# Kernel optimization log

Hardware: AMD Instinct MI355X
Metric: run time of the kernel (lower is better)

## Reference

```python
import jax, jax.numpy as jnp
import numpy as np

T, B, N, C = 4, 4, 4096, 512
H = 8
D = C // H            # head_dim = 64
TAU = 2.0             # LIF tau
VTH = 1.0             # LIF threshold


def lif_spike(x):
    # LIFNode called once from zero state: v = 0 + (x - 0)/tau; spike = v >= vth
    v = x / TAU
    return (v >= VTH).astype(x.dtype)


def setup_inputs() -> dict:
    key = jax.random.key(0)
    ks = jax.random.split(key, 9)
    s = 0.05  # weight scale so pre-spike potentials straddle the threshold
    x = jax.random.normal(ks[0], (T, B, N, C), dtype=jnp.float32)
    Wq = jax.random.normal(ks[1], (C, C), dtype=jnp.float32) * s
    bq = jnp.zeros((C,), dtype=jnp.float32)
    Wk = jax.random.normal(ks[2], (C, C), dtype=jnp.float32) * s
    bk = jnp.zeros((C,), dtype=jnp.float32)
    Wv = jax.random.normal(ks[3], (C, C), dtype=jnp.float32) * s
    bv = jnp.zeros((C,), dtype=jnp.float32)
    Wo = jax.random.normal(ks[4], (C, C), dtype=jnp.float32) * s
    bo = jnp.zeros((C,), dtype=jnp.float32)
    return {"x": x, "Wq": Wq, "bq": bq, "Wk": Wk, "bk": bk,
            "Wv": Wv, "bv": bv, "Wo": Wo, "bo": bo}


def reference(x, Wq, bq, Wk, bk, Wv, bv, Wo, bo):
    # nn.Linear: y = x @ W.T + b (SeqToANNContainer just flattens (T,B))
    q = jnp.einsum('tbnc,oc->tbno', x, Wq) + bq
    k = jnp.einsum('tbnc,oc->tbno', x, Wk) + bk
    v = jnp.einsum('tbnc,oc->tbno', x, Wv) + bv
    # reshape to heads; attention runs over the spiking time axis T per token
    q = q.reshape(T, B, N, H, D).transpose(1, 2, 0, 3, 4)   # (B,N,T,H,D)
    k = k.reshape(T, B, N, H, D).transpose(1, 2, 3, 4, 0)   # (B,N,H,D,T)
    v = v.reshape(T, B, N, H, D).transpose(1, 2, 3, 0, 4)   # (B,N,H,T,D)
    attn = jnp.einsum('bnthd,bnhds->bnths', q, k) / jnp.sqrt(jnp.float32(D))
    attn = lif_spike(attn)                                  # binary spikes replace softmax
    out = jnp.einsum('bnths,bnhsd->bnthd', attn, v)         # (B,N,T,H,D)
    out = out.transpose(2, 0, 1, 3, 4).reshape(T, B, N, C)
    return jnp.einsum('tbnc,oc->tbno', out, Wo) + bo
```

## Files before the change

kernel.cpp:

```cpp
#include <hip/hip_runtime.h>

#define PTOT  16384
#define CCC   512
#define HHH   8
#define NK1   32
#define NK2   16

typedef __attribute__((ext_vector_type(4)))  float f32x4;
typedef __attribute__((ext_vector_type(16))) float f32x16;
typedef _Float16 half_t;
typedef __attribute__((ext_vector_type(8))) _Float16 f16x8;

#define MFMA16(a,b,c) __builtin_amdgcn_mfma_f32_16x16x32_f16(a,b,c,0,0,0)
#define MFMA32(a,b,c) __builtin_amdgcn_mfma_f32_32x32x16_f16(a,b,c,0,0,0)

#define XH_OFF   ((size_t)0)
#define XL_OFF   ((size_t)33554432)
#define ACT_OFF  ((size_t)67108864)
#define W_OFF    ((size_t)100663296)
#define WPL      ((size_t)262144)

__device__ __forceinline__ size_t blk_off16(int row, int col) {
    return ((size_t)((row >> 4) * 16 + (col >> 5)) << 9)
         + (size_t)(((((col >> 3) & 3) * 16) + (row & 15)) << 3) + (col & 7);
}

__global__ void k0_split(const float* __restrict__ x,
                         const float* __restrict__ Wq, const float* __restrict__ Wk,
                         const float* __restrict__ Wv, const float* __restrict__ Wo,
                         half_t* __restrict__ ws)
{
    const int u = blockIdx.x * 256 + threadIdx.x;
    if (u < 4194304) {
        const int f = u >> 6, lane6 = u & 63;
        const int grow32 = f >> 5, ktc = f & 31;
        const int row = grow32 * 32 + (lane6 & 31);
        const int k   = ktc * 16 + (lane6 >> 5) * 8;
        const float4 a = *(const float4*)(x + (size_t)row * CCC + k);
        const float4 b = *(const float4*)(x + (size_t)row * CCC + k + 4);
        const float e[8] = {a.x, a.y, a.z, a.w, b.x, b.y, b.z, b.w};
        f16x8 vh8, vl8;
        #pragma unroll
        for (int d = 0; d < 8; ++d) {
            const half_t hi = (half_t)e[d];
            vh8[d] = hi; vl8[d] = (half_t)(e[d] - (float)hi);
        }
        const size_t off = ((size_t)f << 9) + lane6 * 8;
        *(f16x8*)(ws + XH_OFF + off) = vh8;
        *(f16x8*)(ws + XL_OFF + off) = vl8;
        return;
    }
    const int u2  = u - 4194304;
    const int mat = u2 >> 15, r = u2 & 32767;
    if (mat < 3) {
        const float* src = (mat == 0) ? Wq : (mat == 1) ? Wk : Wv;
        const int f = r >> 6, lane6 = r & 63;
        const int grow32 = f >> 5, ktc = f & 31;
        const int row = grow32 * 32 + (lane6 & 31);
        const int k   = ktc * 16 + (lane6 >> 5) * 8;
        const float4 a = *(const float4*)(src + (size_t)row * CCC + k);
        const float4 b = *(const float4*)(src + (size_t)row * CCC + k + 4);
        const float e[8] = {a.x, a.y, a.z, a.w, b.x, b.y, b.z, b.w};
        f16x8 vh8, vl8;
        #pragma unroll
        for (int d = 0; d < 8; ++d) {
            const half_t hi = (half_t)e[d];
            vh8[d] = hi; vl8[d] = (half_t)(e[d] - (float)hi);
        }
        const size_t off = ((size_t)f << 9) + lane6 * 8;
        half_t* dh = ws + W_OFF + (size_t)(mat * 2) * WPL;
        *(f16x8*)(dh + off) = vh8;
        if (mat < 2) *(f16x8*)(dh + WPL + off) = vl8;
        return;
    }
    const int gr = r >> 10, v = r & 1023;
    const int ktc = v >> 6, chunk = (v >> 4) & 3, i = v & 15;
    const int row = gr * 16 + i, col = ktc * 32 + chunk * 8;
    const float4 a = *(const float4*)(Wo + (size_t)row * CCC + col);
    const float4 b = *(const float4*)(Wo + (size_t)row * CCC + col + 4);
    const float e[8] = {a.x, a.y, a.z, a.w, b.x, b.y, b.z, b.w};
    f16x8 vh8;
    #pragma unroll
    for (int d = 0; d < 8; ++d) vh8[d] = (half_t)e[d];
    *(f16x8*)(ws + W_OFF + 5 * WPL + blk_off16(row, col)) = vh8;
}

__global__ __launch_bounds__(256, 3)
void k1_mfma(const half_t* __restrict__ ws,
             const float* __restrict__ bq, const float* __restrict__ bk,
             const float* __restrict__ bv,
             half_t* __restrict__ acth)
{
    __shared__ __align__(16) char smem[52224];

    const int tid  = threadIdx.x;
    const int lane = tid & 63;
    const int wv   = tid >> 6;
    const int rg   = wv >> 1;
    const int cg   = wv & 1;
    const int l31  = lane & 31;
    const int l5   = lane >> 5;

    const int xcd  = blockIdx.x & 7;
    const int rest = blockIdx.x >> 3;
    const int h    = rest & 7;
    const int tg   = rest >> 3;
    const int p0   = (tg * 8 + xcd) * 32;

    const int cnt  = (wv < 2) ? 5 : 4;
    const int base = (wv < 2) ? wv * 5 : 2 + wv * 4;
    const half_t* gb[5]; int lo_[5];
    #pragma unroll
    for (int ii = 0; ii < 5; ++ii) {
        const int i = base + ii;
        size_t eoff; int loff;
        if (i < 8) {
            const int t = i >> 1, pl = i & 1;
            const size_t rbg = (size_t)t * 512 + (p0 >> 5);
            eoff = (pl ? XL_OFF : XH_OFF) + (rbg << 14) + lane * 8;
            loff = i * 1024;
        } else {
            const int s = (i - 8) & 15;
            const int plw = (s >> 1) > 4 ? 4 : (s >> 1), cb = s & 1;
            eoff = W_OFF + (size_t)plw * WPL + ((size_t)(h * 2 + cb) << 14) + lane * 8;
            loff = 8192 + s * 1024;
        }
        gb[ii] = ws + eoff;
        lo_[ii] = loff;
    }

#define K1_STAGE(buf, kt) do {                                                  \
    _Pragma("unroll")                                                           \
    for (int ii = 0; ii < 5; ++ii)                                              \
        if (ii < cnt)                                                           \
            __builtin_amdgcn_global_load_lds(                                   \
                (const __attribute__((address_space(1))) void*)(gb[ii] + (size_t)(kt) * 512), \
                (__attribute__((address_space(3))) void*)(smem + (buf) * 18432 + lo_[ii]),    \
                16, 0, 0);                                                      \
    } while (0)

    f32x16 accQ[2], accK[2], accV[2];
    {
        const int c0 = h * 64 + cg * 32 + l31;
        const float q0 = bq[c0], k0 = bk[c0], v0 = bv[c0];
        #pragma unroll
        for (int i = 0; i < 16; ++i) {
            accQ[0][i] = q0; accQ[1][i] = q0;
            accK[0][i] = k0; accK[1][i] = k0;
            accV[0][i] = v0; accV[1][i] = v0;
        }
    }

    K1_STAGE(0, 0);

    #pragma unroll 2
    for (int kt = 0; kt < NK1; ++kt) {
        const int cur = kt & 1;
        if (kt + 1 < NK1) {
            K1_STAGE(cur ^ 1, kt + 1);
            if (cnt == 5) asm volatile("s_waitcnt vmcnt(5)" ::: "memory");
            else          asm volatile("s_waitcnt vmcnt(4)" ::: "memory");
        } else {
            asm volatile("s_waitcnt vmcnt(0)" ::: "memory");
        }
        __builtin_amdgcn_sched_barrier(0);
        __builtin_amdgcn_s_barrier();

        const char* bp = smem + cur * 18432;
        const int boff = 8192 + cg * 1024 + lane * 16;
        const int t0 = rg * 2, t1 = rg * 2 + 1;

        const f16x8 Ah0 = *(const f16x8*)(bp + (t0 * 2 + 0) * 1024 + lane * 16);
        const f16x8 Al0 = *(const f16x8*)(bp + (t0 * 2 + 1) * 1024 + lane * 16);
        const f16x8 Ah1 = *(const f16x8*)(bp + (t1 * 2 + 0) * 1024 + lane * 16);
        const f16x8 Al1 = *(const f16x8*)(bp + (t1 * 2 + 1) * 1024 + lane * 16);
        const f16x8 Bqh = *(const f16x8*)(bp + boff);
        const f16x8 Bql = *(const f16x8*)(bp + boff + 2048);
        asm volatile("s_waitcnt lgkmcnt(0)" ::: "memory");
        __builtin_amdgcn_sched_barrier(0);
        __builtin_amdgcn_s_setprio(1);
        accQ[0] = MFMA32(Ah0, Bqh, accQ[0]);
        accQ[1] = MFMA32(Ah1, Bqh, accQ[1]);
        accQ[0] = MFMA32(Ah0, Bql, accQ[0]);
        accQ[1] = MFMA32(Ah1, Bql, accQ[1]);
        accQ[0] = MFMA32(Al0, Bqh, accQ[0]);
        accQ[1] = MFMA32(Al1, Bqh, accQ[1]);
        __builtin_amdgcn_s_setprio(0);
        __builtin_amdgcn_s_barrier();

        const f16x8 Bkh = *(const f16x8*)(bp + boff + 4096);
        const f16x8 Bkl = *(const f16x8*)(bp + boff + 6144);
        const f16x8 Bvh = *(const f16x8*)(bp + boff + 8192);
        asm volatile("s_waitcnt lgkmcnt(0)" ::: "memory");
        __builtin_amdgcn_sched_barrier(0);
        __builtin_amdgcn_s_setprio(1);
        accK[0] = MFMA32(Ah0, Bkh, accK[0]);
        accK[1] = MFMA32(Ah1, Bkh, accK[1]);
        accV[0] = MFMA32(Ah0, Bvh, accV[0]);
        accV[1] = MFMA32(Ah1, Bvh, accV[1]);
        accK[0] = MFMA32(Ah0, Bkl, accK[0]);
        accK[1] = MFMA32(Ah1, Bkl, accK[1]);
        accK[0] = MFMA32(Al0, Bkh, accK[0]);
        accK[1] = MFMA32(Al1, Bkh, accK[1]);
        __builtin_amdgcn_s_setprio(0);
        __builtin_amdgcn_s_barrier();
        __builtin_amdgcn_sched_barrier(0);
    }

    float* qa = (float*)smem;
    float* ka = qa + 4352;
    float* va = qa + 8704;

    const int ar  = tid >> 2;
    const int t_  = ar >> 4;
    const int jj  = ar & 15;
    const int sub = tid & 3;

    #pragma unroll
    for (int hh = 0; hh < 2; ++hh) {
        #pragma unroll
        for (int rf = 0; rf < 2; ++rf) {
            const int t = rg * 2 + rf;
            #pragma unroll
            for (int rr = 0; rr < 8; ++rr) {
                const int reg = hh * 8 + rr;
                const int j2  = (rr & 3) + 8 * (rr >> 2) + 4 * l5;
                const int idx = (t * 16 + j2) * 68 + cg * 32 + l31;
                qa[idx] = accQ[rf][reg];
                ka[idx] = accK[rf][reg];
                va[idx] = accV[rf][reg];
            }
        }
        __syncthreads();

        const float* qp = qa + ar * 68 + sub * 16;
        const float4 q0 = *(const float4*)(qp);
        const float4 q1 = *(const float4*)(qp + 4);
        const float4 q2 = *(const float4*)(qp + 8);
        const float4 q3 = *(const float4*)(qp + 12);
        float sc[4];
        #pragma unroll
        for (int ss = 0; ss < 4; ++ss) {
            const float* kp = ka + (ss * 16 + jj) * 68 + sub * 16;
            const float4 k0 = *(const float4*)(kp);
            const float4 k1 = *(const float4*)(kp + 4);
            const float4 k2 = *(const float4*)(kp + 8);
            const float4 k3 = *(const float4*)(kp + 12);
            float p = q0.x*k0.x + q0.y*k0.y + q0.z*k0.z + q0.w*k0.w
                    + q1.x*k1.x + q1.y*k1.y + q1.z*k1.z + q1.w*k1.w
                    + q2.x*k2.x + q2.y*k2.y + q2.z*k2.z + q2.w*k2.w
                    + q3.x*k3.x + q3.y*k3.y + q3.z*k3.z + q3.w*k3.w;
            p += __shfl_xor(p, 1);
            p += __shfl_xor(p, 2);
            sc[ss] = p;
        }
        float o[16];
        #pragma unroll
        for (int d = 0; d < 16; ++d) o[d] = 0.f;
        #pragma unroll
        for (int ss = 0; ss < 4; ++ss) {
            if (sc[ss] >= 16.0f) {
                const float* vp = va + (ss * 16 + jj) * 68 + sub * 16;
                const float4 v0 = *(const float4*)(vp);
                const float4 v1 = *(const float4*)(vp + 4);
                const float4 v2 = *(const float4*)(vp + 8);
                const float4 v3 = *(const float4*)(vp + 12);
                o[0]+=v0.x; o[1]+=v0.y; o[2]+=v0.z;  o[3]+=v0.w;
                o[4]+=v1.x; o[5]+=v1.y; o[6]+=v1.z;  o[7]+=v1.w;
                o[8]+=v2.x; o[9]+=v2.y; o[10]+=v2.z; o[11]+=v2.w;
                o[12]+=v3.x;o[13]+=v3.y;o[14]+=v3.z; o[15]+=v3.w;
            }
        }
        f16x8 o0, o1;
        #pragma unroll
        for (int d = 0; d < 8; ++d) { o0[d] = (half_t)o[d]; o1[d] = (half_t)o[d + 8]; }
        const int grow = t_ * 1024 + (p0 >> 4) + hh;
        const int colb = h * 64 + sub * 16;
        const size_t cbase = ((size_t)(grow * 16 + (colb >> 5))) << 9;
        const int c0 = (colb >> 3) & 3;
        *(f16x8*)(acth + cbase + (size_t)((c0       * 16 + jj) << 3)) = o0;
        *(f16x8*)(acth + cbase + (size_t)(((c0 + 1) * 16 + jj) << 3)) = o1;
        __syncthreads();
    }
#undef K1_STAGE
}

__global__ __launch_bounds__(256, 4)
void k2_gemm(const half_t* __restrict__ acth, const half_t* __restrict__ oh,
             const float* __restrict__ bo, float* __restrict__ out)
{
    __shared__ __align__(16) char smem[32768];

    const int tid  = threadIdx.x;
    const int lane = tid & 63;
    const int wv   = tid >> 6;
    const int wr   = wv >> 1, wc = wv & 1;
    const int l15  = lane & 15, l4 = lane >> 4;
    const int bn   = (blockIdx.x & 3) * 128;
    const int bm   = (blockIdx.x >> 2) * 128;

    const half_t* gb[4]; int lo_[4];
    #pragma unroll
    for (int ii = 0; ii < 4; ++ii) {
        const int i = wv * 4 + ii;
        if (i < 8) {
            const int grow = (bm >> 4) + i;
            gb[ii] = acth + ((size_t)grow << 13) + lane * 8;
            lo_[ii] = i * 1024;
        } else {
            const int fb = i - 8;
            const int grow = (bn >> 4) + fb;
            gb[ii] = oh + ((size_t)grow << 13) + lane * 8;
            lo_[ii] = 8192 + fb * 1024;
        }
    }

#define K2_STAGE(buf, kt) do {                                                  \
    _Pragma("unroll")                                                           \
    for (int ii = 0; ii < 4; ++ii)                                              \
        __builtin_amdgcn_global_load_lds(                                       \
            (const __attribute__((address_space(1))) void*)(gb[ii] + (size_t)(kt) * 512), \
            (__attribute__((address_space(3))) void*)(smem + (buf) * 16384 + lo_[ii]),    \
            16, 0, 0);                                                          \
    } while (0)

    f32x4 acc[4][4];
    #pragma unroll
    for (int rf = 0; rf < 4; ++rf)
        #pragma unroll
        for (int cf = 0; cf < 4; ++cf) acc[rf][cf] = f32x4{0.f, 0.f, 0.f, 0.f};

    K2_STAGE(0, 0);

    #pragma unroll
    for (int kt = 0; kt < NK2; ++kt) {
        const int cur = kt & 1;
        if (kt + 1 < NK2) {
            K2_STAGE(cur ^ 1, kt + 1);
            asm volatile("s_waitcnt vmcnt(4)" ::: "memory");
        } else {
            asm volatile("s_waitcnt vmcnt(0)" ::: "memory");
        }
        __builtin_amdgcn_sched_barrier(0);
        __builtin_amdgcn_s_barrier();

        const char* bp = smem + cur * 16384;
        f16x8 B[4];
        #pragma unroll
        for (int cf = 0; cf < 4; ++cf)
            B[cf] = *(const f16x8*)(bp + 8192 + (wc * 4 + cf) * 1024 + lane * 16);
        f16x8 A[4];
        #pragma unroll
        for (int rf = 0; rf < 4; ++rf)
            A[rf] = *(const f16x8*)(bp + (wr * 4 + rf) * 1024 + lane * 16);
        asm volatile("s_waitcnt lgkmcnt(0)" ::: "memory");
        __builtin_amdgcn_sched_barrier(0);
        __builtin_amdgcn_s_setprio(1);
        #pragma unroll
        for (int rf = 0; rf < 4; ++rf)
            #pragma unroll
            for (int cf = 0; cf < 4; ++cf)
                acc[rf][cf] = MFMA16(A[rf], B[cf], acc[rf][cf]);
        __builtin_amdgcn_s_setprio(0);
        __builtin_amdgcn_s_barrier();
        __builtin_amdgcn_sched_barrier(0);
    }

    float bo4[4];
    #pragma unroll
    for (int cf = 0; cf < 4; ++cf) bo4[cf] = bo[bn + (wc * 4 + cf) * 16 + l15];

    #pragma unroll
    for (int rf = 0; rf < 4; ++rf) {
        const int row0 = bm + (wr * 4 + rf) * 16 + l4 * 4;
        #pragma unroll
        for (int cf = 0; cf < 4; ++cf) {
            const int col = bn + (wc * 4 + cf) * 16 + l15;
            #pragma unroll
            for (int r = 0; r < 4; ++r)
                out[(size_t)(row0 + r) * CCC + col] = acc[rf][cf][r] + bo4[cf];
        }
    }
#undef K2_STAGE
}

extern "C" void kernel_launch(void* const* d_in, const int* in_sizes, int n_in,
                              void* d_out, int out_size, void* d_ws, size_t ws_size,
                              hipStream_t stream)
{
    const float* x  = (const float*)d_in[0];
    const float* Wq = (const float*)d_in[1];
    const float* bq = (const float*)d_in[2];
    const float* Wk = (const float*)d_in[3];
    const float* bk = (const float*)d_in[4];
    const float* Wv = (const float*)d_in[5];
    const float* bv = (const float*)d_in[6];
    const float* Wo = (const float*)d_in[7];
    const float* bo = (const float*)d_in[8];

    half_t* ws   = (half_t*)d_ws;
    half_t* acth = ws + ACT_OFF;
    float*  out  = (float*)d_out;

    hipLaunchKernelGGL(k0_split, dim3(16896), dim3(256), 0, stream,
                       x, Wq, Wk, Wv, Wo, ws);
    hipLaunchKernelGGL(k1_mfma, dim3(4096), dim3(256), 0, stream,
                       ws, bq, bk, bv, acth);
    hipLaunchKernelGGL(k2_gemm, dim3(2048), dim3(256), 0, stream,
                       acth, ws + W_OFF + 5*WPL, bo, out);
}
```

Baseline: 337.8 us.

## Software-pipeline LDS fragment reads with register double-buffering in both GEMM kernels

Restructures the main loops of the fused QKV kernel and the output projection GEMM. The next stage's LDS fragments are loaded into a second register set while MFMAs consume the current one, and the loop is unrolled by two with explicit waitcnt and barrier placement. This aims to hide LDS read latency behind matrix-core work. It doubles the fragment registers, so k2's launch bounds drop from 4 to 3 waves per SIMD, trading occupancy for pipelining.

```diff
diff --git a/kernel.cpp b/kernel.cpp
--- a/kernel.cpp
+++ b/kernel.cpp
@@ -139,6 +139,13 @@
                 16, 0, 0);                                                      \
     } while (0)
 
+#define VMW_CNT() do { if (cnt == 5) asm volatile("s_waitcnt vmcnt(5)" ::: "memory"); \
+                       else          asm volatile("s_waitcnt vmcnt(4)" ::: "memory"); } while (0)
+#define VMW_0()   asm volatile("s_waitcnt vmcnt(0)" ::: "memory")
+#define LGW_0()   asm volatile("s_waitcnt lgkmcnt(0)" ::: "memory")
+#define SCB()     __builtin_amdgcn_sched_barrier(0)
+#define SBAR()    __builtin_amdgcn_s_barrier()
+
     f32x16 accQ[2], accK[2], accV[2];
     {
         const int c0 = h * 64 + cg * 32 + l31;
@@ -151,62 +158,82 @@
         }
     }
 
+    const int boff = 8192 + cg * 1024 + lane * 16;
+    const int t0 = rg * 2, t1 = rg * 2 + 1;
+    const int aoff0 = (t0 * 2 + 0) * 1024 + lane * 16;
+    const int aoff1 = (t0 * 2 + 1) * 1024 + lane * 16;
+    const int aoff2 = (t1 * 2 + 0) * 1024 + lane * 16;
+    const int aoff3 = (t1 * 2 + 1) * 1024 + lane * 16;
+    const char* bp0 = smem;
+    const char* bp1 = smem + 18432;
+
+    f16x8 A0h0,A0l0,A0h1,A0l1,B0qh,B0ql,B0kh,B0kl,B0vh;
+    f16x8 A1h0,A1l0,A1h1,A1l1,B1qh,B1ql,B1kh,B1kl,B1vh;
+
+#define LOADSET0(bp) do { A0h0=*(const f16x8*)((bp)+aoff0); A0l0=*(const f16x8*)((bp)+aoff1); \
+    A0h1=*(const f16x8*)((bp)+aoff2); A0l1=*(const f16x8*)((bp)+aoff3);                       \
+    B0qh=*(const f16x8*)((bp)+boff); B0ql=*(const f16x8*)((bp)+boff+2048);                    \
+    B0kh=*(const f16x8*)((bp)+boff+4096); B0kl=*(const f16x8*)((bp)+boff+6144);               \
+    B0vh=*(const f16x8*)((bp)+boff+8192); } while (0)
+#define LOADSET1(bp) do { A1h0=*(const f16x8*)((bp)+aoff0); A1l0=*(const f16x8*)((bp)+aoff1); \
+    A1h1=*(const f16x8*)((bp)+aoff2); A1l1=*(const f16x8*)((bp)+aoff3);                       \
+    B1qh=*(const f16x8*)((bp)+boff); B1ql=*(const f16x8*)((bp)+boff+2048);                    \
+    B1kh=*(const f16x8*)((bp)+boff+4096); B1kl=*(const f16x8*)((bp)+boff+6144);               \
+    B1vh=*(const f16x8*)((bp)+boff+8192); } while (0)
+#define MM0() do {                                   \
+    accQ[0]=MFMA32(A0h0,B0qh,accQ[0]); accQ[1]=MFMA32(A0h1,B0qh,accQ[1]);  \
+    accK[0]=MFMA32(A0h0,B0kh,accK[0]); accK[1]=MFMA32(A0h1,B0kh,accK[1]);  \
+    accV[0]=MFMA32(A0h0,B0vh,accV[0]); accV[1]=MFMA32(A0h1,B0vh,accV[1]);  \
+    accQ[0]=MFMA32(A0h0,B0ql,accQ[0]); accQ[1]=MFMA32(A0h1,B0ql,accQ[1]);  \
+    accK[0]=MFMA32(A0h0,B0kl,accK[0]); accK[1]=MFMA32(A0h1,B0kl,accK[1]);  \
+    accQ[0]=MFMA32(A0l0,B0qh,accQ[0]); accQ[1]=MFMA32(A0l1,B0qh,accQ[1]);  \
+    accK[0]=MFMA32(A0l0,B0kh,accK[0]); accK[1]=MFMA32(A0l1,B0kh,accK[1]);  \
+    } while (0)
+#define MM1() do {                                   \
+    accQ[0]=MFMA32(A1h0,B1qh,accQ[0]); accQ[1]=MFMA32(A1h1,B1qh,accQ[1]);  \
+    accK[0]=MFMA32(A1h0,B1kh,accK[0]); accK[1]=MFMA32(A1h1,B1kh,accK[1]);  \
+    accV[0]=MFMA32(A1h0,B1vh,accV[0]); accV[1]=MFMA32(A1h1,B1vh,accV[1]);  \
+    accQ[0]=MFMA32(A1h0,B1ql,accQ[0]); accQ[1]=MFMA32(A1h1,B1ql,accQ[1]);  \
+    accK[0]=MFMA32(A1h0,B1kl,accK[0]); accK[1]=MFMA32(A1h1,B1kl,accK[1]);  \
+    accQ[0]=MFMA32(A1l0,B1qh,accQ[0]); accQ[1]=MFMA32(A1l1,B1qh,accQ[1]);  \
+    accK[0]=MFMA32(A1l0,B1kh,accK[0]); accK[1]=MFMA32(A1l1,B1kh,accK[1]);  \
+    } while (0)
+
     K1_STAGE(0, 0);
-
-    #pragma unroll 2
-    for (int kt = 0; kt < NK1; ++kt) {
-        const int cur = kt & 1;
-        if (kt + 1 < NK1) {
-            K1_STAGE(cur ^ 1, kt + 1);
-            if (cnt == 5) asm volatile("s_waitcnt vmcnt(5)" ::: "memory");
-            else          asm volatile("s_waitcnt vmcnt(4)" ::: "memory");
-        } else {
-            asm volatile("s_waitcnt vmcnt(0)" ::: "memory");
-        }
-        __builtin_amdgcn_sched_barrier(0);
-        __builtin_amdgcn_s_barrier();
-
-        const char* bp = smem + cur * 18432;
-        const int boff = 8192 + cg * 1024 + lane * 16;
-        const int t0 = rg * 2, t1 = rg * 2 + 1;
-
-        const f16x8 Ah0 = *(const f16x8*)(bp + (t0 * 2 + 0) * 1024 + lane * 16);
-        const f16x8 Al0 = *(const f16x8*)(bp + (t0 * 2 + 1) * 1024 + lane * 16);
-        const f16x8 Ah1 = *(const f16x8*)(bp + (t1 * 2 + 0) * 1024 + lane * 16);
-        const f16x8 Al1 = *(const f16x8*)(bp + (t1 * 2 + 1) * 1024 + lane * 16);
-        const f16x8 Bqh = *(const f16x8*)(bp + boff);
-        const f16x8 Bql = *(const f16x8*)(bp + boff + 2048);
-        asm volatile("s_waitcnt lgkmcnt(0)" ::: "memory");
-        __builtin_amdgcn_sched_barrier(0);
+    K1_STAGE(1, 1);
+    VMW_CNT();
+    SCB();
+    SBAR();
+    LOADSET0(bp0);
+
+    #pragma unroll 1
+    for (int kt = 0; kt < NK1; kt += 2) {
+        LGW_0(); SCB();
+        SBAR();
+        if (kt + 2 < NK1) K1_STAGE(0, kt + 2);
+        if (kt + 2 < NK1) { VMW_CNT(); } else { VMW_0(); }
+        SCB();
+        SBAR();
+        LOADSET1(bp1);
         __builtin_amdgcn_s_setprio(1);
-        accQ[0] = MFMA32(Ah0, Bqh, accQ[0]);
-        accQ[1] = MFMA32(Ah1, Bqh, accQ[1]);
-        accQ[0] = MFMA32(Ah0, Bql, accQ[0]);
-        accQ[1] = MFMA32(Ah1, Bql, accQ[1]);
-        accQ[0] = MFMA32(Al0, Bqh, accQ[0]);
-        accQ[1] = MFMA32(Al1, Bqh, accQ[1]);
+        MM0();
         __builtin_amdgcn_s_setprio(0);
-        __builtin_amdgcn_s_barrier();
-
-        const f16x8 Bkh = *(const f16x8*)(bp + boff + 4096);
-        const f16x8 Bkl = *(const f16x8*)(bp + boff + 6144);
-        const f16x8 Bvh = *(const f16x8*)(bp + boff + 8192);
-        asm volatile("s_waitcnt lgkmcnt(0)" ::: "memory");
-        __builtin_amdgcn_sched_barrier(0);
+
+        LGW_0(); SCB();
+        SBAR();
+        if (kt + 3 < NK1) K1_STAGE(1, kt + 3);
+        if (kt + 2 < NK1) {
+            if (kt + 3 < NK1) { VMW_CNT(); } else { VMW_0(); }
+            SCB();
+            SBAR();
+            LOADSET0(bp0);
+        }
         __builtin_amdgcn_s_setprio(1);
-        accK[0] = MFMA32(Ah0, Bkh, accK[0]);
-        accK[1] = MFMA32(Ah1, Bkh, accK[1]);
-        accV[0] = MFMA32(Ah0, Bvh, accV[0]);
-        accV[1] = MFMA32(Ah1, Bvh, accV[1]);
-        accK[0] = MFMA32(Ah0, Bkl, accK[0]);
-        accK[1] = MFMA32(Ah1, Bkl, accK[1]);
-        accK[0] = MFMA32(Al0, Bkh, accK[0]);
-        accK[1] = MFMA32(Al1, Bkh, accK[1]);
+        MM1();
         __builtin_amdgcn_s_setprio(0);
-        __builtin_amdgcn_s_barrier();
-        __builtin_amdgcn_sched_barrier(0);
-    }
-
+    }
+
+    __syncthreads();
     float* qa = (float*)smem;
     float* ka = qa + 4352;
     float* va = qa + 8704;
@@ -283,9 +310,13 @@
         __syncthreads();
     }
 #undef K1_STAGE
+#undef LOADSET0
+#undef LOADSET1
+#undef MM0
+#undef MM1
 }
 
-__global__ __launch_bounds__(256, 4)
+__global__ __launch_bounds__(256, 3)
 void k2_gemm(const half_t* __restrict__ acth, const half_t* __restrict__ oh,
              const float* __restrict__ bo, float* __restrict__ out)
 {
@@ -330,40 +361,73 @@
         #pragma unroll
         for (int cf = 0; cf < 4; ++cf) acc[rf][cf] = f32x4{0.f, 0.f, 0.f, 0.f};
 
+    const char* bp0 = smem;
+    const char* bp1 = smem + 16384;
+    f16x8 A0[4], B0[4], A1[4], B1[4];
+
+#define LOADS2_0(bp) do {                                                      \
+    _Pragma("unroll")                                                          \
+    for (int f = 0; f < 4; ++f) {                                              \
+        A0[f] = *(const f16x8*)((bp) + (wr * 4 + f) * 1024 + lane * 16);       \
+        B0[f] = *(const f16x8*)((bp) + 8192 + (wc * 4 + f) * 1024 + lane * 16);\
+    } } while (0)
+#define LOADS2_1(bp) do {                                                      \
+    _Pragma("unroll")                                                          \
+    for (int f = 0; f < 4; ++f) {                                              \
+        A1[f] = *(const f16x8*)((bp) + (wr * 4 + f) * 1024 + lane * 16);       \
+        B1[f] = *(const f16x8*)((bp) + 8192 + (wc * 4 + f) * 1024 + lane * 16);\
+    } } while (0)
+#define MM2_0() do {                                                           \
+    _Pragma("unroll")                                                          \
+    for (int rf = 0; rf < 4; ++rf)                                             \
+        _Pragma("unroll")                                                      \
+        for (int cf = 0; cf < 4; ++cf)                                         \
+            acc[rf][cf] = MFMA16(A0[rf], B0[cf], acc[rf][cf]);                 \
+    } while (0)
+#define MM2_1() do {                                                           \
+    _Pragma("unroll")                                                          \
+    for (int rf = 0; rf < 4; ++rf)                                             \
+        _Pragma("unroll")                                                      \
+        for (int cf = 0; cf < 4; ++cf)                                         \
+            acc[rf][cf] = MFMA16(A1[rf], B1[cf], acc[rf][cf]);                 \
+    } while (0)
+
     K2_STAGE(0, 0);
-
-    #pragma unroll
-    for (int kt = 0; kt < NK2; ++kt) {
-        const int cur = kt & 1;
-        if (kt + 1 < NK2) {
-            K2_STAGE(cur ^ 1, kt + 1);
-            asm volatile("s_waitcnt vmcnt(4)" ::: "memory");
-        } else {
-            asm volatile("s_waitcnt vmcnt(0)" ::: "memory");
-        }
+    K2_STAGE(1, 1);
+    asm volatile("s_waitcnt vmcnt(4)" ::: "memory");
+    __builtin_amdgcn_sched_barrier(0);
+    __builtin_amdgcn_s_barrier();
+    LOADS2_0(bp0);
+
+    #pragma unroll 1
+    for (int kt = 0; kt < NK2; kt += 2) {
+        asm volatile("s_waitcnt lgkmcnt(0)" ::: "memory");
         __builtin_amdgcn_sched_barrier(0);
         __builtin_amdgcn_s_barrier();
-
-        const char* bp = smem + cur * 16384;
-        f16x8 B[4];
-        #pragma unroll
-        for (int cf = 0; cf < 4; ++cf)
-            B[cf] = *(const f16x8*)(bp + 8192 + (wc * 4 + cf) * 1024 + lane * 16);
-        f16x8 A[4];
-        #pragma unroll
-        for (int rf = 0; rf < 4; ++rf)
-            A[rf] = *(const f16x8*)(bp + (wr * 4 + rf) * 1024 + lane * 16);
+        if (kt + 2 < NK2) K2_STAGE(0, kt + 2);
+        if (kt + 2 < NK2) asm volatile("s_waitcnt vmcnt(4)" ::: "memory");
+        else              asm volatile("s_waitcnt vmcnt(0)" ::: "memory");
+        __builtin_amdgcn_sched_barrier(0);
+        __builtin_amdgcn_s_barrier();
+        LOADS2_1(bp1);
+        __builtin_amdgcn_s_setprio(1);
+        MM2_0();
+        __builtin_amdgcn_s_setprio(0);
+
         asm volatile("s_waitcnt lgkmcnt(0)" ::: "memory");
         __builtin_amdgcn_sched_barrier(0);
+        __builtin_amdgcn_s_barrier();
+        if (kt + 3 < NK2) K2_STAGE(1, kt + 3);
+        if (kt + 2 < NK2) {
+            if (kt + 3 < NK2) asm volatile("s_waitcnt vmcnt(4)" ::: "memory");
+            else              asm volatile("s_waitcnt vmcnt(0)" ::: "memory");
+            __builtin_amdgcn_sched_barrier(0);
+            __builtin_amdgcn_s_barrier();
+            LOADS2_0(bp0);
+        }
         __builtin_amdgcn_s_setprio(1);
-        #pragma unroll
-        for (int rf = 0; rf < 4; ++rf)
-            #pragma unroll
-            for (int cf = 0; cf < 4; ++cf)
-                acc[rf][cf] = MFMA16(A[rf], B[cf], acc[rf][cf]);
+        MM2_1();
         __builtin_amdgcn_s_setprio(0);
-        __builtin_amdgcn_s_barrier();
-        __builtin_amdgcn_sched_barrier(0);
     }
 
     float bo4[4];
@@ -382,6 +446,10 @@
         }
     }
 #undef K2_STAGE
+#undef LOADS2_0
+#undef LOADS2_1
+#undef MM2_0
+#undef MM2_1
 }
 
 extern "C" void kernel_launch(void* const* d_in, const int* in_sizes, int n_in,
```

Result: slower. 974.4 us (+188.5%).
